# Optimization experiments

Measured on AMD Instinct MI355X. Metric: run time of the kernel, lower is better.

Reference implementation:

```python
import jax, jax.numpy as jnp
import numpy as np

N = 100000      # nodes
E = 1600000     # edges
D_IN = 100
D_OUT = 100


def _sage(x, src, dst, W_agg, W_root, b):
    """PyG SAGEConv, aggr='mean', root_weight=True:
    out = mean_{j in N(i)} x_j @ W_agg + x_i @ W_root + b
    Aggregation flows source -> target (dst gathers from src)."""
    num_nodes = x.shape[0]
    deg = jax.ops.segment_sum(jnp.ones((src.shape[0],), x.dtype), dst,
                              num_segments=num_nodes)
    agg = jax.ops.segment_sum(x[src], dst, num_segments=num_nodes)  # [N, D]
    agg = agg / jnp.maximum(deg, 1.0)[:, None]
    return agg @ W_agg + x @ W_root + b


def setup_inputs() -> dict:
    key = jax.random.key(0)
    ks = jax.random.split(key, 12)
    s = 0.05
    return {
        "x": jax.random.normal(ks[0], (N, D_IN), jnp.float32),
        "edge_index": jax.random.randint(ks[1], (2, E), 0, N, jnp.int32),
        "edge_weight": jax.random.uniform(ks[2], (E,), jnp.float32),
        "W_sage_agg": jax.random.normal(ks[3], (D_IN, D_OUT), jnp.float32) * s,
        "W_sage_root": jax.random.normal(ks[4], (D_IN, D_OUT), jnp.float32) * s,
        "b_sage": jnp.zeros((D_OUT,), jnp.float32),
        "W_mu_agg": jax.random.normal(ks[5], (D_OUT, D_OUT), jnp.float32) * s,
        "W_mu_root": jax.random.normal(ks[6], (D_OUT, D_OUT), jnp.float32) * s,
        "b_mu": jnp.zeros((D_OUT,), jnp.float32),
        "W_var_agg": jax.random.normal(ks[7], (D_OUT, D_OUT), jnp.float32) * s,
        "W_var_root": jax.random.normal(ks[8], (D_OUT, D_OUT), jnp.float32) * s,
        "b_var": jnp.zeros((D_OUT,), jnp.float32),
    }


def reference(x, edge_index, edge_weight,
              W_sage_agg, W_sage_root, b_sage,
              W_mu_agg, W_mu_root, b_mu,
              W_var_agg, W_var_root, b_var):
    # edge_weight is accepted but unused, matching the torch module.
    src, dst = edge_index[0], edge_index[1]
    feat = jax.nn.relu(_sage(x, src, dst, W_sage_agg, W_sage_root, b_sage))
    mu = _sage(feat, src, dst, W_mu_agg, W_mu_root, b_mu)
    var = _sage(feat, src, dst, W_var_agg, W_var_root, b_var)
    return (mu, var)
```

## Files before the change

kernel.cpp:

```cpp
#include <hip/hip_runtime.h>
#include <cstdint>
#include <cstddef>

#define N_NODES 100000
#define N_EDGES 1600000
#define DIM 100
#define DPAD 128
#define ROWS_ALLOC 100096

#define KBUCK 500
#define NPB   200
#define BCAP  4096
#define EPB   6400

typedef __attribute__((ext_vector_type(8))) short s16x8;
typedef __attribute__((ext_vector_type(8))) unsigned short us8;
typedef __attribute__((ext_vector_type(4))) unsigned short us4;
typedef __attribute__((ext_vector_type(4))) float f32x4;

static __device__ __forceinline__ float bf2f(unsigned short h) {
    return __uint_as_float(((unsigned)h) << 16);
}
static __device__ __forceinline__ unsigned short f2bf(float f) {
    unsigned u = __float_as_uint(f);
    return (unsigned short)((u + 0x7FFFu + ((u >> 16) & 1u)) >> 16);
}

__global__ __launch_bounds__(256) void bucket_kernel(const int* __restrict__ ei,
                                                     unsigned* __restrict__ bucket_cur,
                                                     unsigned* __restrict__ regions) {
    __shared__ unsigned hist[KBUCK];
    __shared__ unsigned posl[KBUCK];
    int tid = threadIdx.x;
    int e0 = blockIdx.x * EPB;
    for (int i = tid; i < KBUCK; i += 256) hist[i] = 0;
    __syncthreads();
    for (int i = tid; i < EPB; i += 256) {
        int dst = ei[N_EDGES + e0 + i];
        int b = dst / NPB;
        atomicAdd(&hist[b], 1u);
    }
    __syncthreads();
    for (int i = tid; i < KBUCK; i += 256) {
        unsigned h = hist[i];
        posl[i] = h ? atomicAdd(&bucket_cur[i], h) : 0u;
    }
    __syncthreads();
    for (int i = tid; i < EPB; i += 256) {
        int src = ei[e0 + i];
        int dst = ei[N_EDGES + e0 + i];
        int b = dst / NPB;
        int dl = dst - b * NPB;
        unsigned r = atomicAdd(&posl[b], 1u);
        if (r < BCAP) regions[(size_t)b * BCAP + r] = ((unsigned)src << 8) | (unsigned)dl;
    }
}

__global__ __launch_bounds__(256) void csr_kernel(const unsigned* __restrict__ regions,
                                                  const unsigned* __restrict__ bucket_cur,
                                                  unsigned* __restrict__ gbase,
                                                  int* __restrict__ row_off,
                                                  int* __restrict__ cnt,
                                                  int* __restrict__ csr_src) {
    __shared__ unsigned hist[256];
    __shared__ unsigned sa[256], sb[256];
    __shared__ unsigned posl[256];
    __shared__ unsigned sh_gb;
    int tid = threadIdx.x;
    int b = blockIdx.x;
    unsigned total = bucket_cur[b];
    if (total > BCAP) total = BCAP;
    hist[tid] = 0;
    __syncthreads();
    const unsigned* reg = regions + (size_t)b * BCAP;
    for (unsigned e = tid; e < total; e += 256)
        atomicAdd(&hist[reg[e] & 0xFFu], 1u);
    __syncthreads();
    unsigned* cur = sa; unsigned* nxt = sb;
    cur[tid] = hist[tid];
    __syncthreads();
    for (int off = 1; off < 256; off <<= 1) {
        unsigned t = cur[tid];
        if (tid >= off) t += cur[tid - off];
        nxt[tid] = t;
        __syncthreads();
        unsigned* tmp = cur; cur = nxt; nxt = tmp;
    }
    unsigned excl = cur[tid] - hist[tid];
    if (tid == 0) sh_gb = atomicAdd(gbase, total);
    __syncthreads();
    unsigned gb = sh_gb;
    posl[tid] = gb + excl;
    if (tid < NPB) {
        int node = b * NPB + tid;
        cnt[node] = (int)hist[tid];
        row_off[node] = (int)(gb + excl);
    }
    __syncthreads();
    for (unsigned e = tid; e < total; e += 256) {
        unsigned p = reg[e];
        unsigned r = atomicAdd(&posl[p & 0xFFu], 1u);
        csr_src[r] = (int)(p >> 8);
    }
}

__global__ __launch_bounds__(256) void convert_pad(const float* __restrict__ X,
                                                   unsigned short* __restrict__ Xp) {
    int t = blockIdx.x * 256 + threadIdx.x;
    if (t >= N_NODES * 16) return;
    int node = t >> 4, chunk = t & 15;
    us8 o;
    if (chunk < 12) {
        const float4* p = (const float4*)(X + (size_t)node * DIM + chunk * 8);
        float4 a = p[0], b = p[1];
        o[0] = f2bf(a.x); o[1] = f2bf(a.y); o[2] = f2bf(a.z); o[3] = f2bf(a.w);
        o[4] = f2bf(b.x); o[5] = f2bf(b.y); o[6] = f2bf(b.z); o[7] = f2bf(b.w);
    } else if (chunk == 12) {
        const float4* p = (const float4*)(X + (size_t)node * DIM + 96);
        float4 a = p[0];
        o[0] = f2bf(a.x); o[1] = f2bf(a.y); o[2] = f2bf(a.z); o[3] = f2bf(a.w);
        o[4] = 0; o[5] = 0; o[6] = 0; o[7] = 0;
    } else {
        for (int i = 0; i < 8; ++i) o[i] = 0;
    }
    *(us8*)(Xp + (size_t)node * DPAD + chunk * 8) = o;
}

__global__ __launch_bounds__(256) void build_w(const float* __restrict__ W0, const float* __restrict__ W1,
                                               const float* __restrict__ W2, const float* __restrict__ W3,
                                               const float* __restrict__ W4, const float* __restrict__ W5,
                                               unsigned short* __restrict__ Wt) {
    int t = blockIdx.x * 256 + threadIdx.x;
    if (t >= 6 * DPAD * 16) return;
    int mat = t / (DPAD * 16);
    int rem = t % (DPAD * 16);
    int nrow = rem >> 4, chunk = rem & 15;
    const float* W = (mat == 0) ? W0 : (mat == 1) ? W1 : (mat == 2) ? W2
                   : (mat == 3) ? W3 : (mat == 4) ? W4 : W5;
    us8 o;
    #pragma unroll
    for (int j = 0; j < 8; ++j) {
        int k = chunk * 8 + j;
        float v = (k < DIM && nrow < DIM) ? W[(size_t)k * DIM + nrow] : 0.f;
        o[j] = f2bf(v);
    }
    *(us8*)(Wt + (size_t)mat * DPAD * DPAD + (size_t)nrow * DPAD + chunk * 8) = o;
}

__global__ __launch_bounds__(256) void build_bias(const float* __restrict__ b0, const float* __restrict__ b1,
                                                  const float* __restrict__ b2, float* __restrict__ bp) {
    int t = blockIdx.x * 256 + threadIdx.x;
    if (t >= 3 * DPAD) return;
    int mat = t / DPAD, i = t % DPAD;
    const float* b = (mat == 0) ? b0 : (mat == 1) ? b1 : b2;
    bp[t] = (i < DIM) ? b[i] : 0.f;
}

__global__ __launch_bounds__(256) void aggregate_pad(const unsigned short* __restrict__ Xh,
                                                     const int* __restrict__ csr_src,
                                                     const int* __restrict__ row_off,
                                                     const int* __restrict__ cnt,
                                                     unsigned short* __restrict__ outh, int n) {
    int node = blockIdx.x * 4 + (threadIdx.x >> 6);
    if (node >= n) return;
    int lane = threadIdx.x & 63;
    int chunk = lane & 15;
    int slot  = lane >> 4;
    int start = row_off[node];
    int deg   = cnt[node];
    float acc[8];
    #pragma unroll
    for (int i = 0; i < 8; ++i) acc[i] = 0.f;
    for (int base = 0; base < deg; base += 64) {
        int m = deg - base; if (m > 64) m = 64;
        int sv = (lane < m) ? csr_src[start + base + lane] : 0;
        #pragma unroll 4
        for (int j = 0; j < m; j += 4) {
            int s = __shfl(sv, j + slot, 64);
            if (j + slot < m) {
                us8 u = *(const us8*)(Xh + (size_t)s * DPAD + chunk * 8);
                #pragma unroll
                for (int i = 0; i < 8; ++i) acc[i] += bf2f(u[i]);
            }
        }
    }
    #pragma unroll
    for (int i = 0; i < 8; ++i) {
        acc[i] += __shfl_xor(acc[i], 16, 64);
        acc[i] += __shfl_xor(acc[i], 32, 64);
    }
    if (lane < 16) {
        float inv = 1.0f / (float)(deg > 0 ? deg : 1);
        us8 o;
        #pragma unroll
        for (int i = 0; i < 8; ++i) o[i] = f2bf(acc[i] * inv);
        *(us8*)(outh + (size_t)node * DPAD + chunk * 8) = o;
    }
}

__global__ __launch_bounds__(256) void gemm_l1_strip(const unsigned short* __restrict__ Aagg,
                                                     const unsigned short* __restrict__ Aroot,
                                                     const unsigned short* __restrict__ WtA,
                                                     const unsigned short* __restrict__ WtR,
                                                     const float* __restrict__ bpad,
                                                     unsigned short* __restrict__ outp) {
    int lane  = threadIdx.x & 63;
    int strip = threadIdx.x >> 6;
    int m16   = lane & 15;
    int quad  = lane >> 4;
    int row0  = blockIdx.x * 64;

    s16x8 wf[2][2][4];
    const unsigned short* Ws[2] = {WtA, WtR};
    #pragma unroll
    for (int ph = 0; ph < 2; ++ph)
        #pragma unroll
        for (int nt = 0; nt < 2; ++nt)
            #pragma unroll
            for (int ks = 0; ks < 4; ++ks)
                wf[ph][nt][ks] = *(const s16x8*)(Ws[ph] + (size_t)(strip * 32 + nt * 16 + m16) * DPAD + ks * 32 + quad * 8);

    float4 bias4[2];
    #pragma unroll
    for (int nt = 0; nt < 2; ++nt)
        bias4[nt] = *(const float4*)(bpad + strip * 32 + nt * 16 + quad * 4);

    #pragma unroll
    for (int t = 0; t < 4; ++t) {
        int m = row0 + t * 16 + m16;
        s16x8 afA[4], afR[4];
        #pragma unroll
        for (int ks = 0; ks < 4; ++ks) {
            afA[ks] = *(const s16x8*)(Aagg  + (size_t)m * DPAD + ks * 32 + quad * 8);
            afR[ks] = *(const s16x8*)(Aroot + (size_t)m * DPAD + ks * 32 + quad * 8);
        }
        f32x4 acc[2];
        acc[0] = (f32x4){0.f, 0.f, 0.f, 0.f};
        acc[1] = (f32x4){0.f, 0.f, 0.f, 0.f};
        #pragma unroll
        for (int ks = 0; ks < 4; ++ks) {
            acc[0] = __builtin_amdgcn_mfma_f32_16x16x32_bf16(wf[0][0][ks], afA[ks], acc[0], 0, 0, 0);
            acc[1] = __builtin_amdgcn_mfma_f32_16x16x32_bf16(wf[0][1][ks], afA[ks], acc[1], 0, 0, 0);
            acc[0] = __builtin_amdgcn_mfma_f32_16x16x32_bf16(wf[1][0][ks], afR[ks], acc[0], 0, 0, 0);
            acc[1] = __builtin_amdgcn_mfma_f32_16x16x32_bf16(wf[1][1][ks], afR[ks], acc[1], 0, 0, 0);
        }
        #pragma unroll
        for (int nt = 0; nt < 2; ++nt) {
            int col0 = strip * 32 + nt * 16 + quad * 4;
            us4 o;
            #pragma unroll
            for (int r = 0; r < 4; ++r) {
                float v = acc[nt][r] + ((const float*)&bias4[nt])[r];
                v = v > 0.f ? v : 0.f;
                o[r] = f2bf(v);
            }
            *(us4*)(outp + (size_t)m * DPAD + col0) = o;
        }
    }
}

__global__ __launch_bounds__(256) void gemm_l2_strip(const unsigned short* __restrict__ Aagg,
                                                     const unsigned short* __restrict__ Afeat,
                                                     const unsigned short* __restrict__ WtMA,
                                                     const unsigned short* __restrict__ WtMR,
                                                     const unsigned short* __restrict__ WtVA,
                                                     const unsigned short* __restrict__ WtVR,
                                                     const float* __restrict__ bpm,
                                                     const float* __restrict__ bpv,
                                                     float* __restrict__ outMu,
                                                     float* __restrict__ outVar) {
    int lane  = threadIdx.x & 63;
    int strip = threadIdx.x >> 6;
    int m16   = lane & 15;
    int quad  = lane >> 4;
    int row0  = blockIdx.x * 64;

    s16x8 wf[2][2][2][4];
    const unsigned short* Ws[2][2] = {{WtMA, WtMR}, {WtVA, WtVR}};
    #pragma unroll
    for (int hd = 0; hd < 2; ++hd)
        #pragma unroll
        for (int ph = 0; ph < 2; ++ph)
            #pragma unroll
            for (int nt = 0; nt < 2; ++nt)
                #pragma unroll
                for (int ks = 0; ks < 4; ++ks)
                    wf[hd][ph][nt][ks] = *(const s16x8*)(Ws[hd][ph] + (size_t)(strip * 32 + nt * 16 + m16) * DPAD + ks * 32 + quad * 8);

    float4 bm4[2], bv4[2];
    #pragma unroll
    for (int nt = 0; nt < 2; ++nt) {
        bm4[nt] = *(const float4*)(bpm + strip * 32 + nt * 16 + quad * 4);
        bv4[nt] = *(const float4*)(bpv + strip * 32 + nt * 16 + quad * 4);
    }

    #pragma unroll
    for (int t = 0; t < 4; ++t) {
        int m = row0 + t * 16 + m16;
        s16x8 afA[4], afF[4];
        #pragma unroll
        for (int ks = 0; ks < 4; ++ks) {
            afA[ks] = *(const s16x8*)(Aagg  + (size_t)m * DPAD + ks * 32 + quad * 8);
            afF[ks] = *(const s16x8*)(Afeat + (size_t)m * DPAD + ks * 32 + quad * 8);
        }
        f32x4 aM[2], aV[2];
        aM[0] = (f32x4){0.f,0.f,0.f,0.f}; aM[1] = (f32x4){0.f,0.f,0.f,0.f};
        aV[0] = (f32x4){0.f,0.f,0.f,0.f}; aV[1] = (f32x4){0.f,0.f,0.f,0.f};
        #pragma unroll
        for (int ks = 0; ks < 4; ++ks) {
            aM[0] = __builtin_amdgcn_mfma_f32_16x16x32_bf16(wf[0][0][0][ks], afA[ks], aM[0], 0, 0, 0);
            aM[1] = __builtin_amdgcn_mfma_f32_16x16x32_bf16(wf[0][0][1][ks], afA[ks], aM[1], 0, 0, 0);
            aV[0] = __builtin_amdgcn_mfma_f32_16x16x32_bf16(wf[1][0][0][ks], afA[ks], aV[0], 0, 0, 0);
            aV[1] = __builtin_amdgcn_mfma_f32_16x16x32_bf16(wf[1][0][1][ks], afA[ks], aV[1], 0, 0, 0);
            aM[0] = __builtin_amdgcn_mfma_f32_16x16x32_bf16(wf[0][1][0][ks], afF[ks], aM[0], 0, 0, 0);
            aM[1] = __builtin_amdgcn_mfma_f32_16x16x32_bf16(wf[0][1][1][ks], afF[ks], aM[1], 0, 0, 0);
            aV[0] = __builtin_amdgcn_mfma_f32_16x16x32_bf16(wf[1][1][0][ks], afF[ks], aV[0], 0, 0, 0);
            aV[1] = __builtin_amdgcn_mfma_f32_16x16x32_bf16(wf[1][1][1][ks], afF[ks], aV[1], 0, 0, 0);
        }
        if (m < N_NODES) {
            #pragma unroll
            for (int nt = 0; nt < 2; ++nt) {
                int col0 = strip * 32 + nt * 16 + quad * 4;
                if (col0 <= DIM - 4) {
                    float4 vm, vv;
                    vm.x = aM[nt][0] + bm4[nt].x; vm.y = aM[nt][1] + bm4[nt].y;
                    vm.z = aM[nt][2] + bm4[nt].z; vm.w = aM[nt][3] + bm4[nt].w;
                    vv.x = aV[nt][0] + bv4[nt].x; vv.y = aV[nt][1] + bv4[nt].y;
                    vv.z = aV[nt][2] + bv4[nt].z; vv.w = aV[nt][3] + bv4[nt].w;
                    *(float4*)(outMu  + (size_t)m * DIM + col0) = vm;
                    *(float4*)(outVar + (size_t)m * DIM + col0) = vv;
                }
            }
        }
    }
}

extern "C" void kernel_launch(void* const* d_in, const int* in_sizes, int n_in,
                              void* d_out, int out_size, void* d_ws, size_t ws_size,
                              hipStream_t stream) {
    const float* x   = (const float*)d_in[0];
    const int*   ei  = (const int*)d_in[1];
    const float* Wsa = (const float*)d_in[3];
    const float* Wsr = (const float*)d_in[4];
    const float* bs  = (const float*)d_in[5];
    const float* Wma = (const float*)d_in[6];
    const float* Wmr = (const float*)d_in[7];
    const float* bm  = (const float*)d_in[8];
    const float* Wva = (const float*)d_in[9];
    const float* Wvr = (const float*)d_in[10];
    const float* bv  = (const float*)d_in[11];

    float* out_mu  = (float*)d_out;
    float* out_var = out_mu + (size_t)N_NODES * DIM;

    char* ws = (char*)d_ws;
    int*      row_off    = (int*)(ws);
    int*      cnt        = (int*)(ws + 400000);
    unsigned* bucket_cur = (unsigned*)(ws + 800000);
    unsigned* gbase      = (unsigned*)(ws + 802048);
    int*      csr_src    = (int*)(ws + 802176);
    unsigned short* Wt   = (unsigned short*)(ws + 7202176);
    float*          bp   = (float*)(ws + 7398784);
    unsigned short* xp   = (unsigned short*)(ws + 7400448);
    unsigned short* aggp = (unsigned short*)(ws + 33025024);
    unsigned short* ftp  = (unsigned short*)(ws + 58649600);
    unsigned* regions    = (unsigned*)(ws + 7400448);

    unsigned short* WtSA = Wt;
    unsigned short* WtSR = Wt + 1 * DPAD * DPAD;
    unsigned short* WtMA = Wt + 2 * DPAD * DPAD;
    unsigned short* WtMR = Wt + 3 * DPAD * DPAD;
    unsigned short* WtVA = Wt + 4 * DPAD * DPAD;
    unsigned short* WtVR = Wt + 5 * DPAD * DPAD;
    float* bps = bp;
    float* bpm = bp + DPAD;
    float* bpv = bp + 2 * DPAD;

    hipMemsetAsync(bucket_cur, 0, 2048, stream);
    hipMemsetAsync(gbase, 0, 128, stream);

    bucket_kernel<<<N_EDGES / EPB, 256, 0, stream>>>(ei, bucket_cur, regions);
    csr_kernel<<<KBUCK, 256, 0, stream>>>(regions, bucket_cur, gbase, row_off, cnt, csr_src);

    convert_pad<<<(N_NODES * 16 + 255) / 256, 256, 0, stream>>>(x, xp);
    build_w<<<(6 * DPAD * 16 + 255) / 256, 256, 0, stream>>>(Wsa, Wsr, Wma, Wmr, Wva, Wvr, Wt);
    build_bias<<<2, 256, 0, stream>>>(bs, bm, bv, bp);

    aggregate_pad<<<N_NODES / 4, 256, 0, stream>>>(xp, csr_src, row_off, cnt, aggp, N_NODES);
    gemm_l1_strip<<<ROWS_ALLOC / 64, 256, 0, stream>>>(aggp, xp, WtSA, WtSR, bps, ftp);

    aggregate_pad<<<N_NODES / 4, 256, 0, stream>>>(ftp, csr_src, row_off, cnt, aggp, N_NODES);
    gemm_l2_strip<<<ROWS_ALLOC / 64, 256, 0, stream>>>(aggp, ftp, WtMA, WtMR, WtVA, WtVR,
                                                       bpm, bpv, out_mu, out_var);
}
```

Baseline: 420.3 us.

## Fuse mean aggregation with MFMA GEMM per layer via swizzled LDS tile

Merges the separate aggregate and GEMM kernels of each SAGE layer into one kernel. Each block first aggregates 64 nodes into a bank-swizzled shared-memory tile, then runs the bf16 MFMA GEMM straight from LDS, so the intermediate agg buffer never goes to global memory. The gather loop is also restructured so each lane issues four independent neighbour-row loads with masked accumulation, and layer 2 processes the mu and var heads in turn to cut register pressure. In exchange, occupancy is limited by LDS and the launch bound, and the GEMM phase can only start after the block's slowest aggregation finishes.

```diff
diff --git a/kernel.cpp b/kernel.cpp
--- a/kernel.cpp
+++ b/kernel.cpp
@@ -8,6 +8,9 @@
 #define DPAD 128
 #define ROWS_ALLOC 100096
 
+#define FRPB 64
+#define FGRID (ROWS_ALLOC / FRPB)
+
 #define KBUCK 500
 #define NPB   200
 #define BCAP  4096
@@ -17,6 +20,8 @@
 typedef __attribute__((ext_vector_type(8))) unsigned short us8;
 typedef __attribute__((ext_vector_type(4))) unsigned short us4;
 typedef __attribute__((ext_vector_type(4))) float f32x4;
+typedef __attribute__((ext_vector_type(2))) float f32x2;
+typedef __attribute__((ext_vector_type(4))) unsigned int u32x4;
 
 static __device__ __forceinline__ float bf2f(unsigned short h) {
     return __uint_as_float(((unsigned)h) << 16);
@@ -156,59 +161,89 @@
     bp[t] = (i < DIM) ? b[i] : 0.f;
 }
 
-__global__ __launch_bounds__(256) void aggregate_pad(const unsigned short* __restrict__ Xh,
-                                                     const int* __restrict__ csr_src,
-                                                     const int* __restrict__ row_off,
-                                                     const int* __restrict__ cnt,
-                                                     unsigned short* __restrict__ outh, int n) {
-    int node = blockIdx.x * 4 + (threadIdx.x >> 6);
-    if (node >= n) return;
-    int lane = threadIdx.x & 63;
-    int chunk = lane & 15;
-    int slot  = lane >> 4;
-    int start = row_off[node];
-    int deg   = cnt[node];
-    float acc[8];
-    #pragma unroll
-    for (int i = 0; i < 8; ++i) acc[i] = 0.f;
-    for (int base = 0; base < deg; base += 64) {
-        int m = deg - base; if (m > 64) m = 64;
-        int sv = (lane < m) ? csr_src[start + base + lane] : 0;
-        #pragma unroll 4
-        for (int j = 0; j < m; j += 4) {
-            int s = __shfl(sv, j + slot, 64);
-            if (j + slot < m) {
-                us8 u = *(const us8*)(Xh + (size_t)s * DPAD + chunk * 8);
+
+static __device__ __forceinline__ void agg_node(const unsigned short* __restrict__ Xh,
+                                                const int* __restrict__ csr_src,
+                                                int start, int deg, int slot, int coff,
+                                                f32x2 acc2[4]) {
+    const int* ep = csr_src + start;
+    for (int base = 0; base < deg; base += 16) {
+        int sarr[4]; float msk[4];
+        #pragma unroll
+        for (int i = 0; i < 4; ++i) {
+            int el = base + slot * 4 + i;
+            sarr[i] = ep[el < deg ? el : deg - 1];
+            msk[i]  = el < deg ? 1.f : 0.f;
+        }
+        u32x4 w[4];
+        #pragma unroll
+        for (int i = 0; i < 4; ++i)
+            w[i] = *(const u32x4*)(Xh + (size_t)sarr[i] * DPAD + coff);
+        #pragma unroll
+        for (int i = 0; i < 4; ++i) {
+            f32x2 mm = (f32x2){msk[i], msk[i]};
+            #pragma unroll
+            for (int k = 0; k < 4; ++k) {
+                f32x2 v = (f32x2){__uint_as_float(w[i][k] << 16), __uint_as_float(w[i][k] & 0xFFFF0000u)};
+                acc2[k] += v * mm;
+            }
+        }
+    }
+}
+
+__global__ __launch_bounds__(256, 3) void fused_l1(const unsigned short* __restrict__ Xh,
+                                                   const int* __restrict__ csr_src,
+                                                   const int* __restrict__ row_off,
+                                                   const int* __restrict__ cnt,
+                                                   const unsigned short* __restrict__ WtA,
+                                                   const unsigned short* __restrict__ WtR,
+                                                   const float* __restrict__ bpad,
+                                                   unsigned short* __restrict__ outp) {
+    __shared__ unsigned short aggT[FRPB * DPAD];
+    int tid  = threadIdx.x;
+    int lane = tid & 63;
+    int wid  = tid >> 6;
+    int row0 = blockIdx.x * FRPB;
+
+    {
+        int chunk = lane & 15;
+        int slot  = lane >> 4;
+        const int coff = chunk * 8;
+        for (int i = 0; i < 16; ++i) {
+            int lrow = wid * 16 + i;
+            int node = row0 + lrow;
+            int start = 0, deg = 0;
+            if (node < N_NODES) { start = row_off[node]; deg = cnt[node]; }
+            f32x2 acc2[4];
+            #pragma unroll
+            for (int k = 0; k < 4; ++k) acc2[k] = (f32x2){0.f, 0.f};
+            agg_node(Xh, csr_src, start, deg, slot, coff, acc2);
+            #pragma unroll
+            for (int k = 0; k < 4; ++k) {
+                acc2[k].x += __shfl_xor(acc2[k].x, 16, 64);
+                acc2[k].y += __shfl_xor(acc2[k].y, 16, 64);
+                acc2[k].x += __shfl_xor(acc2[k].x, 32, 64);
+                acc2[k].y += __shfl_xor(acc2[k].y, 32, 64);
+            }
+            if (lane < 16) {
+                float inv = 1.0f / (float)(deg > 0 ? deg : 1);
+                us8 o;
                 #pragma unroll
-                for (int i = 0; i < 8; ++i) acc[i] += bf2f(u[i]);
-            }
-        }
-    }
-    #pragma unroll
-    for (int i = 0; i < 8; ++i) {
-        acc[i] += __shfl_xor(acc[i], 16, 64);
-        acc[i] += __shfl_xor(acc[i], 32, 64);
-    }
-    if (lane < 16) {
-        float inv = 1.0f / (float)(deg > 0 ? deg : 1);
-        us8 o;
-        #pragma unroll
-        for (int i = 0; i < 8; ++i) o[i] = f2bf(acc[i] * inv);
-        *(us8*)(outh + (size_t)node * DPAD + chunk * 8) = o;
-    }
-}
-
-__global__ __launch_bounds__(256) void gemm_l1_strip(const unsigned short* __restrict__ Aagg,
-                                                     const unsigned short* __restrict__ Aroot,
-                                                     const unsigned short* __restrict__ WtA,
-                                                     const unsigned short* __restrict__ WtR,
-                                                     const float* __restrict__ bpad,
-                                                     unsigned short* __restrict__ outp) {
-    int lane  = threadIdx.x & 63;
-    int strip = threadIdx.x >> 6;
+                for (int k = 0; k < 4; ++k) {
+                    o[2 * k]     = f2bf(acc2[k].x * inv);
+                    o[2 * k + 1] = f2bf(acc2[k].y * inv);
+                }
+                int byte = lrow * 256 + chunk * 16;
+                byte ^= (lrow & 7) << 4;
+                *(us8*)((char*)aggT + byte) = o;
+            }
+        }
+    }
+    __syncthreads();
+
+    int strip = wid;
     int m16   = lane & 15;
     int quad  = lane >> 4;
-    int row0  = blockIdx.x * 64;
 
     s16x8 wf[2][2][4];
     const unsigned short* Ws[2] = {WtA, WtR};
@@ -226,24 +261,27 @@
         bias4[nt] = *(const float4*)(bpad + strip * 32 + nt * 16 + quad * 4);
 
     #pragma unroll
-    for (int t = 0; t < 4; ++t) {
-        int m = row0 + t * 16 + m16;
-        s16x8 afA[4], afR[4];
+    for (int t = 0; t < FRPB / 16; ++t) {
+        int lrow = t * 16 + m16;
+        s16x8 aA[4], aR[4];
         #pragma unroll
         for (int ks = 0; ks < 4; ++ks) {
-            afA[ks] = *(const s16x8*)(Aagg  + (size_t)m * DPAD + ks * 32 + quad * 8);
-            afR[ks] = *(const s16x8*)(Aroot + (size_t)m * DPAD + ks * 32 + quad * 8);
+            int byte = lrow * 256 + ks * 64 + quad * 16;
+            byte ^= (lrow & 7) << 4;
+            aA[ks] = *(const s16x8*)((char*)aggT + byte);
+            aR[ks] = *(const s16x8*)(Xh + (size_t)(row0 + lrow) * DPAD + ks * 32 + quad * 8);
         }
         f32x4 acc[2];
         acc[0] = (f32x4){0.f, 0.f, 0.f, 0.f};
         acc[1] = (f32x4){0.f, 0.f, 0.f, 0.f};
         #pragma unroll
         for (int ks = 0; ks < 4; ++ks) {
-            acc[0] = __builtin_amdgcn_mfma_f32_16x16x32_bf16(wf[0][0][ks], afA[ks], acc[0], 0, 0, 0);
-            acc[1] = __builtin_amdgcn_mfma_f32_16x16x32_bf16(wf[0][1][ks], afA[ks], acc[1], 0, 0, 0);
-            acc[0] = __builtin_amdgcn_mfma_f32_16x16x32_bf16(wf[1][0][ks], afR[ks], acc[0], 0, 0, 0);
-            acc[1] = __builtin_amdgcn_mfma_f32_16x16x32_bf16(wf[1][1][ks], afR[ks], acc[1], 0, 0, 0);
-        }
+            acc[0] = __builtin_amdgcn_mfma_f32_16x16x32_bf16(wf[0][0][ks], aA[ks], acc[0], 0, 0, 0);
+            acc[1] = __builtin_amdgcn_mfma_f32_16x16x32_bf16(wf[0][1][ks], aA[ks], acc[1], 0, 0, 0);
+            acc[0] = __builtin_amdgcn_mfma_f32_16x16x32_bf16(wf[1][0][ks], aR[ks], acc[0], 0, 0, 0);
+            acc[1] = __builtin_amdgcn_mfma_f32_16x16x32_bf16(wf[1][1][ks], aR[ks], acc[1], 0, 0, 0);
+        }
+        int m = row0 + t * 16 + m16;
         #pragma unroll
         for (int nt = 0; nt < 2; ++nt) {
             int col0 = strip * 32 + nt * 16 + quad * 4;
@@ -259,76 +297,116 @@
     }
 }
 
-__global__ __launch_bounds__(256) void gemm_l2_strip(const unsigned short* __restrict__ Aagg,
-                                                     const unsigned short* __restrict__ Afeat,
-                                                     const unsigned short* __restrict__ WtMA,
-                                                     const unsigned short* __restrict__ WtMR,
-                                                     const unsigned short* __restrict__ WtVA,
-                                                     const unsigned short* __restrict__ WtVR,
-                                                     const float* __restrict__ bpm,
-                                                     const float* __restrict__ bpv,
-                                                     float* __restrict__ outMu,
-                                                     float* __restrict__ outVar) {
-    int lane  = threadIdx.x & 63;
-    int strip = threadIdx.x >> 6;
+__global__ __launch_bounds__(256, 3) void fused_l2(const unsigned short* __restrict__ Fh,
+                                                   const int* __restrict__ csr_src,
+                                                   const int* __restrict__ row_off,
+                                                   const int* __restrict__ cnt,
+                                                   const unsigned short* __restrict__ WtMA,
+                                                   const unsigned short* __restrict__ WtMR,
+                                                   const unsigned short* __restrict__ WtVA,
+                                                   const unsigned short* __restrict__ WtVR,
+                                                   const float* __restrict__ bpm,
+                                                   const float* __restrict__ bpv,
+                                                   float* __restrict__ outMu,
+                                                   float* __restrict__ outVar) {
+    __shared__ unsigned short aggT[FRPB * DPAD];
+    int tid  = threadIdx.x;
+    int lane = tid & 63;
+    int wid  = tid >> 6;
+    int row0 = blockIdx.x * FRPB;
+
+    {
+        int chunk = lane & 15;
+        int slot  = lane >> 4;
+        const int coff = chunk * 8;
+        for (int i = 0; i < 16; ++i) {
+            int lrow = wid * 16 + i;
+            int node = row0 + lrow;
+            int start = 0, deg = 0;
+            if (node < N_NODES) { start = row_off[node]; deg = cnt[node]; }
+            f32x2 acc2[4];
+            #pragma unroll
+            for (int k = 0; k < 4; ++k) acc2[k] = (f32x2){0.f, 0.f};
+            agg_node(Fh, csr_src, start, deg, slot, coff, acc2);
+            #pragma unroll
+            for (int k = 0; k < 4; ++k) {
+                acc2[k].x += __shfl_xor(acc2[k].x, 16, 64);
+                acc2[k].y += __shfl_xor(acc2[k].y, 16, 64);
+                acc2[k].x += __shfl_xor(acc2[k].x, 32, 64);
+                acc2[k].y += __shfl_xor(acc2[k].y, 32, 64);
+            }
+            if (lane < 16) {
+                float inv = 1.0f / (float)(deg > 0 ? deg : 1);
+                us8 o;
+                #pragma unroll
+                for (int k = 0; k < 4; ++k) {
+                    o[2 * k]     = f2bf(acc2[k].x * inv);
+                    o[2 * k + 1] = f2bf(acc2[k].y * inv);
+                }
+                int byte = lrow * 256 + chunk * 16;
+                byte ^= (lrow & 7) << 4;
+                *(us8*)((char*)aggT + byte) = o;
+            }
+        }
+    }
+    __syncthreads();
+
+    int strip = wid;
     int m16   = lane & 15;
     int quad  = lane >> 4;
-    int row0  = blockIdx.x * 64;
-
-    s16x8 wf[2][2][2][4];
-    const unsigned short* Ws[2][2] = {{WtMA, WtMR}, {WtVA, WtVR}};
+
+    const unsigned short* WsA[2] = {WtMA, WtVA};
+    const unsigned short* WsR[2] = {WtMR, WtVR};
+    const float* bbs[2] = {bpm, bpv};
+    float* outs[2] = {outMu, outVar};
+
     #pragma unroll
-    for (int hd = 0; hd < 2; ++hd)
-        #pragma unroll
-        for (int ph = 0; ph < 2; ++ph)
-            #pragma unroll
-            for (int nt = 0; nt < 2; ++nt)
+    for (int hd = 0; hd < 2; ++hd) {
+        s16x8 wf[2][2][4];
+        #pragma unroll
+        for (int nt = 0; nt < 2; ++nt)
+            #pragma unroll
+            for (int ks = 0; ks < 4; ++ks) {
+                wf[0][nt][ks] = *(const s16x8*)(WsA[hd] + (size_t)(strip * 32 + nt * 16 + m16) * DPAD + ks * 32 + quad * 8);
+                wf[1][nt][ks] = *(const s16x8*)(WsR[hd] + (size_t)(strip * 32 + nt * 16 + m16) * DPAD + ks * 32 + quad * 8);
+            }
+        float4 b4[2];
+        #pragma unroll
+        for (int nt = 0; nt < 2; ++nt)
+            b4[nt] = *(const float4*)(bbs[hd] + strip * 32 + nt * 16 + quad * 4);
+
+        #pragma unroll
+        for (int t = 0; t < FRPB / 16; ++t) {
+            int lrow = t * 16 + m16;
+            s16x8 aA[4], aF[4];
+            #pragma unroll
+            for (int ks = 0; ks < 4; ++ks) {
+                int byte = lrow * 256 + ks * 64 + quad * 16;
+                byte ^= (lrow & 7) << 4;
+                aA[ks] = *(const s16x8*)((char*)aggT + byte);
+                aF[ks] = *(const s16x8*)(Fh + (size_t)(row0 + lrow) * DPAD + ks * 32 + quad * 8);
+            }
+            f32x4 acc[2];
+            acc[0] = (f32x4){0.f, 0.f, 0.f, 0.f};
+            acc[1] = (f32x4){0.f, 0.f, 0.f, 0.f};
+            #pragma unroll
+            for (int ks = 0; ks < 4; ++ks) {
+                acc[0] = __builtin_amdgcn_mfma_f32_16x16x32_bf16(wf[0][0][ks], aA[ks], acc[0], 0, 0, 0);
+                acc[1] = __builtin_amdgcn_mfma_f32_16x16x32_bf16(wf[0][1][ks], aA[ks], acc[1], 0, 0, 0);
+                acc[0] = __builtin_amdgcn_mfma_f32_16x16x32_bf16(wf[1][0][ks], aF[ks], acc[0], 0, 0, 0);
+                acc[1] = __builtin_amdgcn_mfma_f32_16x16x32_bf16(wf[1][1][ks], aF[ks], acc[1], 0, 0, 0);
+            }
+            int m = row0 + t * 16 + m16;
+            if (m < N_NODES) {
                 #pragma unroll
-                for (int ks = 0; ks < 4; ++ks)
-                    wf[hd][ph][nt][ks] = *(const s16x8*)(Ws[hd][ph] + (size_t)(strip * 32 + nt * 16 + m16) * DPAD + ks * 32 + quad * 8);
-
-    float4 bm4[2], bv4[2];
-    #pragma unroll
-    for (int nt = 0; nt < 2; ++nt) {
-        bm4[nt] = *(const float4*)(bpm + strip * 32 + nt * 16 + quad * 4);
-        bv4[nt] = *(const float4*)(bpv + strip * 32 + nt * 16 + quad * 4);
-    }
-
-    #pragma unroll
-    for (int t = 0; t < 4; ++t) {
-        int m = row0 + t * 16 + m16;
-        s16x8 afA[4], afF[4];
-        #pragma unroll
-        for (int ks = 0; ks < 4; ++ks) {
-            afA[ks] = *(const s16x8*)(Aagg  + (size_t)m * DPAD + ks * 32 + quad * 8);
-            afF[ks] = *(const s16x8*)(Afeat + (size_t)m * DPAD + ks * 32 + quad * 8);
-        }
-        f32x4 aM[2], aV[2];
-        aM[0] = (f32x4){0.f,0.f,0.f,0.f}; aM[1] = (f32x4){0.f,0.f,0.f,0.f};
-        aV[0] = (f32x4){0.f,0.f,0.f,0.f}; aV[1] = (f32x4){0.f,0.f,0.f,0.f};
-        #pragma unroll
-        for (int ks = 0; ks < 4; ++ks) {
-            aM[0] = __builtin_amdgcn_mfma_f32_16x16x32_bf16(wf[0][0][0][ks], afA[ks], aM[0], 0, 0, 0);
-            aM[1] = __builtin_amdgcn_mfma_f32_16x16x32_bf16(wf[0][0][1][ks], afA[ks], aM[1], 0, 0, 0);
-            aV[0] = __builtin_amdgcn_mfma_f32_16x16x32_bf16(wf[1][0][0][ks], afA[ks], aV[0], 0, 0, 0);
-            aV[1] = __builtin_amdgcn_mfma_f32_16x16x32_bf16(wf[1][0][1][ks], afA[ks], aV[1], 0, 0, 0);
-            aM[0] = __builtin_amdgcn_mfma_f32_16x16x32_bf16(wf[0][1][0][ks], afF[ks], aM[0], 0, 0, 0);
-            aM[1] = __builtin_amdgcn_mfma_f32_16x16x32_bf16(wf[0][1][1][ks], afF[ks], aM[1], 0, 0, 0);
-            aV[0] = __builtin_amdgcn_mfma_f32_16x16x32_bf16(wf[1][1][0][ks], afF[ks], aV[0], 0, 0, 0);
-            aV[1] = __builtin_amdgcn_mfma_f32_16x16x32_bf16(wf[1][1][1][ks], afF[ks], aV[1], 0, 0, 0);
-        }
-        if (m < N_NODES) {
-            #pragma unroll
-            for (int nt = 0; nt < 2; ++nt) {
-                int col0 = strip * 32 + nt * 16 + quad * 4;
-                if (col0 <= DIM - 4) {
-                    float4 vm, vv;
-                    vm.x = aM[nt][0] + bm4[nt].x; vm.y = aM[nt][1] + bm4[nt].y;
-                    vm.z = aM[nt][2] + bm4[nt].z; vm.w = aM[nt][3] + bm4[nt].w;
-                    vv.x = aV[nt][0] + bv4[nt].x; vv.y = aV[nt][1] + bv4[nt].y;
-                    vv.z = aV[nt][2] + bv4[nt].z; vv.w = aV[nt][3] + bv4[nt].w;
-                    *(float4*)(outMu  + (size_t)m * DIM + col0) = vm;
-                    *(float4*)(outVar + (size_t)m * DIM + col0) = vv;
+                for (int nt = 0; nt < 2; ++nt) {
+                    int col0 = strip * 32 + nt * 16 + quad * 4;
+                    if (col0 <= DIM - 4) {
+                        float4 vo;
+                        vo.x = acc[nt][0] + b4[nt].x; vo.y = acc[nt][1] + b4[nt].y;
+                        vo.z = acc[nt][2] + b4[nt].z; vo.w = acc[nt][3] + b4[nt].w;
+                        *(float4*)(outs[hd] + (size_t)m * DIM + col0) = vo;
+                    }
                 }
             }
         }
@@ -362,8 +440,7 @@
     unsigned short* Wt   = (unsigned short*)(ws + 7202176);
     float*          bp   = (float*)(ws + 7398784);
     unsigned short* xp   = (unsigned short*)(ws + 7400448);
-    unsigned short* aggp = (unsigned short*)(ws + 33025024);
-    unsigned short* ftp  = (unsigned short*)(ws + 58649600);
+    unsigned short* ftp  = (unsigned short*)(ws + 33025024);
     unsigned* regions    = (unsigned*)(ws + 7400448);
 
     unsigned short* WtSA = Wt;
@@ -386,10 +463,8 @@
     build_w<<<(6 * DPAD * 16 + 255) / 256, 256, 0, stream>>>(Wsa, Wsr, Wma, Wmr, Wva, Wvr, Wt);
     build_bias<<<2, 256, 0, stream>>>(bs, bm, bv, bp);
 
-    aggregate_pad<<<N_NODES / 4, 256, 0, stream>>>(xp, csr_src, row_off, cnt, aggp, N_NODES);
-    gemm_l1_strip<<<ROWS_ALLOC / 64, 256, 0, stream>>>(aggp, xp, WtSA, WtSR, bps, ftp);
-
-    aggregate_pad<<<N_NODES / 4, 256, 0, stream>>>(ftp, csr_src, row_off, cnt, aggp, N_NODES);
-    gemm_l2_strip<<<ROWS_ALLOC / 64, 256, 0, stream>>>(aggp, ftp, WtMA, WtMR, WtVA, WtVR,
-                                                       bpm, bpv, out_mu, out_var);
-}
+    fused_l1<<<FGRID, 256, 0, stream>>>(xp, csr_src, row_off, cnt, WtSA, WtSR, bps, ftp);
+
+    fused_l2<<<FGRID, 256, 0, stream>>>(ftp, csr_src, row_off, cnt, WtMA, WtMR, WtVA, WtVR,
+                                        bpm, bpv, out_mu, out_var);
+}
```

Measured after the change: 430.0 us. 1.02x slower.
